# Kernel optimization log

Measured on AMD Instinct MI355X. Metric: run time of the kernel, lower is better.

## Reference

```python
import jax, jax.numpy as jnp
import numpy as np

NUM_ITER = 3  # routing iterations (canonical CapsNet)
EPS = 1e-12


def _conv(x, w, stride):
    return jax.lax.conv_general_dilated(
        x, w, (stride, stride), 'VALID',
        dimension_numbers=('NCHW', 'OIHW', 'NCHW'))


def _squash(t, axis=-1):
    sn = (t * t).sum(axis=axis, keepdims=True)
    return sn / (1.0 + sn) * t / jnp.sqrt(sn + EPS)


def _batchnorm(x, eps=1e-5):
    # fresh BatchNorm2d in training mode: batch stats, weight=1, bias=0, biased var
    m = x.mean((0, 2, 3), keepdims=True)
    v = ((x - m) ** 2).mean((0, 2, 3), keepdims=True)
    return (x - m) * jax.lax.rsqrt(v + eps)


def _branch(x, cw, cb, pw, pb, rw):
    # x: [B,1,H,W]; cw: [128,1,k,k]; pw: [8,32,128,k,k]; rw: [10,R,8,16]
    y = jax.nn.relu(_conv(x, cw, 1) + cb[None, :, None, None])
    y = _batchnorm(y)
    nc, oc = pw.shape[0], pw.shape[1]  # 8 capsules, 32 channels each
    p = _conv(y, pw.reshape(nc * oc, pw.shape[2], pw.shape[3], pw.shape[4]), 2)
    p = p + pb.reshape(-1)[None, :, None, None]          # [B,256,h,w]
    B = p.shape[0]
    u = jnp.transpose(p.reshape(B, nc, -1), (0, 2, 1))   # [B,R,8], R=32*h*w
    u = _squash(u, axis=-1)
    priors = jnp.einsum('bri,nrio->nbro', u, rw)         # [10,B,R,16]
    b = jnp.zeros(priors.shape[:3] + (1,), priors.dtype)  # [10,B,R,1]
    for i in range(NUM_ITER):
        c = jax.nn.softmax(b, axis=2)                    # over route nodes
        v = _squash((c * priors).sum(axis=2, keepdims=True))  # [10,B,1,16]
        if i < NUM_ITER - 1:
            b = b + (priors * v).sum(axis=-1, keepdims=True)
    v = jnp.transpose(v[:, :, 0, :], (1, 0, 2))          # [B,10,16]
    return jnp.sqrt((v * v).sum(-1) + EPS)               # [B,10] capsule lengths


def setup_inputs() -> dict:
    key = jax.random.key(0)
    ks = jax.random.split(key, 16)
    s = 0.05
    return {
        'x': jax.random.normal(ks[0], (256, 1, 28, 28), jnp.float32),
        'conv1_w': jax.random.normal(ks[1], (128, 1, 3, 3), jnp.float32) * s,
        'conv1_b': jnp.zeros((128,), jnp.float32),
        'prim1_w': jax.random.normal(ks[2], (8, 32, 128, 3, 3), jnp.float32) * s,
        'prim1_b': jnp.zeros((8, 32), jnp.float32),
        'digit1_w': jax.random.normal(ks[3], (10, 128, 8, 16), jnp.float32),
        'conv2_w': jax.random.normal(ks[4], (128, 1, 5, 5), jnp.float32) * s,
        'conv2_b': jnp.zeros((128,), jnp.float32),
        'prim2_w': jax.random.normal(ks[5], (8, 32, 128, 5, 5), jnp.float32) * s,
        'prim2_b': jnp.zeros((8, 32), jnp.float32),
        'digit2_w': jax.random.normal(ks[6], (10, 288, 8, 16), jnp.float32),
        'conv3_w': jax.random.normal(ks[7], (128, 1, 9, 9), jnp.float32) * s,
        'conv3_b': jnp.zeros((128,), jnp.float32),
        'prim3_w': jax.random.normal(ks[8], (8, 32, 128, 9, 9), jnp.float32) * s,
        'prim3_b': jnp.zeros((8, 32), jnp.float32),
        'digit3_w': jax.random.normal(ks[9], (10, 1152, 8, 16), jnp.float32),
    }


def reference(x, conv1_w, conv1_b, prim1_w, prim1_b, digit1_w,
              conv2_w, conv2_b, prim2_w, prim2_b, digit2_w,
              conv3_w, conv3_b, prim3_w, prim3_b, digit3_w):
    img = x[:, 0]                                   # [B,28,28]
    B = img.shape[0]
    x3 = img                                        # 28x28
    x2 = img.reshape(B, 14, 2, 14, 2).mean((2, 4))  # 14x14 pyramid level
    x1 = x2.reshape(B, 7, 2, 7, 2).mean((2, 4))     # 7x7 pyramid level
    l1 = _branch(x1[:, None], conv1_w, conv1_b, prim1_w, prim1_b, digit1_w)
    l2 = _branch(x2[:, None], conv2_w, conv2_b, prim2_w, prim2_b, digit2_w)
    l3 = _branch(x3[:, None], conv3_w, conv3_b, prim3_w, prim3_b, digit3_w)
    return jax.nn.softmax(l1 + l2 + l3, axis=-1)    # [B,10]
```

## Files before the change

kernel.cpp:

```cpp
#include <hip/hip_runtime.h>
#include <math.h>

#define SQ_EPS 1e-12f
#define BN_EPS 1e-5f

typedef short short8 __attribute__((ext_vector_type(8)));
typedef float f32x4 __attribute__((ext_vector_type(4)));
typedef unsigned short ushort_t;

__device__ inline unsigned short f2bf(float x) {
    unsigned int u = __float_as_uint(x);
    unsigned int r = (u + 0x7fffu + ((u >> 16) & 1u)) >> 16;
    return (unsigned short)r;
}
__device__ inline float bf2f(unsigned short h) {
    return __uint_as_float(((unsigned int)h) << 16);
}

template<int IH, int IW, int KS, int OH, int OW>
__device__ void conv_body(const float* __restrict__ w, const float* __restrict__ bias,
                          ushort_t* __restrict__ yh, ushort_t* __restrict__ yl,
                          float* __restrict__ partial,
                          int b, int tid, float* s_img, float* s_w, float* s_red) {
    constexpr int KK = KS * KS;
    constexpr int OS = OH * OW;
    for (int i = tid; i < 128 * KK; i += 256) s_w[i] = w[i];
    __syncthreads();
    int c = tid & 127, half = tid >> 7;
    float bias_c = bias[c];
    float bsum = 0.f, bsq = 0.f;
    for (int r = half; r < OH; r += 2) {
        float acc[OW];
        #pragma unroll
        for (int j = 0; j < OW; ++j) acc[j] = bias_c;
        for (int u = 0; u < KS; ++u) {
            float rg[OW + KS - 1];
            #pragma unroll
            for (int j = 0; j < OW + KS - 1; ++j) rg[j] = s_img[(r + u) * IW + j];
            #pragma unroll
            for (int v = 0; v < KS; ++v) {
                float wv = s_w[c * KK + u * KS + v];
                #pragma unroll
                for (int j = 0; j < OW; ++j) acc[j] += wv * rg[j + v];
            }
        }
        #pragma unroll
        for (int j = 0; j < OW; ++j) {
            float val = fmaxf(acc[j], 0.f);
            bsum += val; bsq += val * val;
            unsigned short h = f2bf(val);
            unsigned short lo = f2bf(val - bf2f(h));
            int oidx = ((b * OS) + r * OW + j) * 128 + c;
            yh[oidx] = h; yl[oidx] = lo;
        }
    }
    s_red[tid] = bsum; __syncthreads();
    if (tid < 128) partial[b * 256 + c] = s_red[tid] + s_red[tid + 128];
    __syncthreads();
    s_red[tid] = bsq; __syncthreads();
    if (tid < 128) partial[b * 256 + 128 + c] = s_red[tid] + s_red[tid + 128];
}

__global__ __launch_bounds__(256) void conv_all_kernel(
        const float* __restrict__ img,
        const float* __restrict__ c1w, const float* __restrict__ c1b,
        const float* __restrict__ c2w, const float* __restrict__ c2b,
        const float* __restrict__ c3w, const float* __restrict__ c3b,
        ushort_t* __restrict__ yh1, ushort_t* __restrict__ yl1,
        ushort_t* __restrict__ yh2, ushort_t* __restrict__ yl2,
        ushort_t* __restrict__ yh3, ushort_t* __restrict__ yl3,
        float* __restrict__ partial_base) {
    __shared__ float s_img[784];
    __shared__ float s_tmp[196];
    __shared__ float s_w[128 * 81];
    __shared__ float s_red[256];
    int br = blockIdx.x >> 8, b = blockIdx.x & 255, tid = threadIdx.x;
    const float* im = img + b * 784;
    for (int i = tid; i < 784; i += 256) s_img[i] = im[i];
    __syncthreads();
    if (br <= 1) {
        for (int idx = tid; idx < 196; idx += 256) {
            int i = idx / 14, j = idx % 14;
            s_tmp[idx] = 0.25f * (s_img[(2*i)*28 + 2*j]   + s_img[(2*i)*28 + 2*j + 1] +
                                  s_img[(2*i+1)*28 + 2*j] + s_img[(2*i+1)*28 + 2*j + 1]);
        }
        __syncthreads();
        if (br == 0) {
            for (int idx = tid; idx < 49; idx += 256) {
                int i = idx / 7, j = idx % 7;
                s_img[idx] = 0.25f * (s_tmp[(2*i)*14 + 2*j]   + s_tmp[(2*i)*14 + 2*j + 1] +
                                      s_tmp[(2*i+1)*14 + 2*j] + s_tmp[(2*i+1)*14 + 2*j + 1]);
            }
        } else {
            for (int idx = tid; idx < 196; idx += 256) s_img[idx] = s_tmp[idx];
        }
        __syncthreads();
    }
    if (br == 0)      conv_body<7, 7, 3, 5, 5>(c1w, c1b, yh1, yl1, partial_base, b, tid, s_img, s_w, s_red);
    else if (br == 1) conv_body<14, 14, 5, 10, 10>(c2w, c2b, yh2, yl2, partial_base + 65536, b, tid, s_img, s_w, s_red);
    else              conv_body<28, 28, 9, 20, 20>(c3w, c3b, yh3, yl3, partial_base + 131072, b, tid, s_img, s_w, s_red);
}

__global__ void bn_final_kernel(const float* __restrict__ partial_base, float* __restrict__ bnp_base) {
    int br = blockIdx.x;
    const float* pp = partial_base + br * 65536;
    float* bnp = bnp_base + br * 512;
    float N = (br == 0) ? 6400.f : ((br == 1) ? 25600.f : 102400.f);
    int c = threadIdx.x;
    float s = 0.f, q = 0.f;
    for (int blk = 0; blk < 256; ++blk) {
        s += pp[blk * 256 + c];
        q += pp[blk * 256 + 128 + c];
    }
    float mean = s / N;
    float var = q / N - mean * mean;
    float inv = rsqrtf(var + BN_EPS);
    bnp[256 + c] = inv;
    bnp[384 + c] = -mean * inv;
}

__global__ __launch_bounds__(256) void wtrans_zero_kernel(
        const float* __restrict__ w1, const float* __restrict__ w2,
        const float* __restrict__ w3, const float* __restrict__ bnp_base,
        const float* __restrict__ pb1, const float* __restrict__ pb2,
        const float* __restrict__ pb3,
        ushort_t* __restrict__ wh1, ushort_t* __restrict__ wl1,
        ushort_t* __restrict__ wh2, ushort_t* __restrict__ wl2,
        ushort_t* __restrict__ wh3, ushort_t* __restrict__ wl3,
        float* __restrict__ b1, float* __restrict__ b2, float* __restrict__ b3,
        float* __restrict__ p3zero) {
    __shared__ float tile[128 * 81];
    __shared__ float r2[2];
    int blk = blockIdx.x, tid = threadIdx.x;
    if (blk >= 768) {
        ((float4*)p3zero)[(blk - 768) * 256 + tid] = (float4){0.f, 0.f, 0.f, 0.f};
        return;
    }
    int br = blk >> 8, ch = blk & 255;
    const float* w; const float* pb; ushort_t* wh; ushort_t* wl; float* bf; int KK;
    if (br == 0)      { w = w1; pb = pb1; wh = wh1; wl = wl1; bf = b1; KK = 9;  }
    else if (br == 1) { w = w2; pb = pb2; wh = wh2; wl = wl2; bf = b2; KK = 25; }
    else              { w = w3; pb = pb3; wh = wh3; wl = wl3; bf = b3; KK = 81; }
    const float* bnp = bnp_base + br * 512;
    int n = 128 * KK;
    const float* wrow = w + ch * n;
    for (int i = tid; i < n; i += 256) tile[i] = wrow[i];
    __syncthreads();
    for (int j = tid; j < n; j += 256) {
        int uv = j >> 7, c = j & 127;
        float val = tile[c * KK + uv] * bnp[256 + c];
        unsigned short h = f2bf(val);
        unsigned short lo = f2bf(val - bf2f(h));
        int oidx = uv * 32768 + (ch << 7) + c;
        wh[oidx] = h; wl[oidx] = lo;
    }
    float s = 0.f;
    if (tid < 128) {
        for (int uv = 0; uv < KK; ++uv) s += tile[tid * KK + uv];
        s *= bnp[384 + tid];
    }
    for (int off = 32; off; off >>= 1) s += __shfl_down(s, off);
    if (tid < 128 && (tid & 63) == 0) r2[tid >> 6] = s;
    __syncthreads();
    if (tid == 0) bf[ch] = pb[ch] + r2[0] + r2[1];
}

template<int S, int WO, int IHg, int IWg, int KS, int ZCH>
__device__ void gemm_body(const ushort_t* __restrict__ yh, const ushort_t* __restrict__ yl,
                          const ushort_t* __restrict__ wh, const ushort_t* __restrict__ wl,
                          float* __restrict__ p, int bx, int by, int bz, int tid,
                          ushort_t* Ash, ushort_t* Asl, ushort_t* Bsh, ushort_t* Bsl) {
    int bm = bx * 128, ch0 = by * 128;
    int arow = tid >> 2;
    int c0 = tid & 3;
    int sw0 = (c0 ^ ((arow >> 1) & 3)) * 8;
    int wA0 = arow * 32 + sw0;
    int wA1 = (arow + 64) * 32 + sw0;
    int m0 = bm + arow;
    int b0 = m0 / S, s0 = m0 % S;
    int abase0 = ((b0 * IHg + 2 * (s0 / WO)) * IWg + 2 * (s0 % WO)) * 128 + c0 * 8;
    int m1 = m0 + 64;
    int b1 = m1 / S, s1 = m1 % S;
    int abase1 = ((b1 * IHg + 2 * (s1 / WO)) * IWg + 2 * (s1 % WO)) * 128 + c0 * 8;
    int bbase0 = (ch0 + arow) * 128 + c0 * 8;
    int bbase1 = (ch0 + arow + 64) * 128 + c0 * 8;
    int lane = tid & 63, wid = tid >> 6;
    int wm = wid & 1, wn = wid >> 1;
    int quad = lane >> 4, l16 = lane & 15;
    int aoffL[4], boffL[4];
    #pragma unroll
    for (int mi = 0; mi < 4; ++mi) {
        int row = wm * 64 + mi * 16 + l16;
        aoffL[mi] = row * 32 + ((quad ^ ((row >> 1) & 3)) * 8);
    }
    #pragma unroll
    for (int ni = 0; ni < 4; ++ni) {
        int row = wn * 64 + ni * 16 + l16;
        boffL[ni] = row * 32 + ((quad ^ ((row >> 1) & 3)) * 8);
    }
    f32x4 acc[4][4];
    #pragma unroll
    for (int mi = 0; mi < 4; ++mi)
        #pragma unroll
        for (int ni = 0; ni < 4; ++ni)
            acc[mi][ni] = (f32x4){0.f, 0.f, 0.f, 0.f};

    int kc = bz * ZCH;
    int uv = kc >> 2, ci = kc & 3;
    int u = uv / KS, v = uv - u * KS;
    int aoff = (u * IWg + v) * 128 + (ci << 5);
    int boff = uv * 32768 + (ci << 5);
    int4 a0h = *reinterpret_cast<const int4*>(yh + abase0 + aoff);
    int4 a0l = *reinterpret_cast<const int4*>(yl + abase0 + aoff);
    int4 a1h = *reinterpret_cast<const int4*>(yh + abase1 + aoff);
    int4 a1l = *reinterpret_cast<const int4*>(yl + abase1 + aoff);
    int4 b0h = *reinterpret_cast<const int4*>(wh + bbase0 + boff);
    int4 b0l = *reinterpret_cast<const int4*>(wl + bbase0 + boff);
    int4 b1h = *reinterpret_cast<const int4*>(wh + bbase1 + boff);
    int4 b1l = *reinterpret_cast<const int4*>(wl + bbase1 + boff);

    for (int t = 0; t < ZCH; ++t) {
        __syncthreads();
        *reinterpret_cast<int4*>(&Ash[wA0]) = a0h;
        *reinterpret_cast<int4*>(&Asl[wA0]) = a0l;
        *reinterpret_cast<int4*>(&Ash[wA1]) = a1h;
        *reinterpret_cast<int4*>(&Asl[wA1]) = a1l;
        *reinterpret_cast<int4*>(&Bsh[wA0]) = b0h;
        *reinterpret_cast<int4*>(&Bsl[wA0]) = b0l;
        *reinterpret_cast<int4*>(&Bsh[wA1]) = b1h;
        *reinterpret_cast<int4*>(&Bsl[wA1]) = b1l;
        if (t + 1 < ZCH) {
            ci = (ci + 1) & 3;
            if (ci == 0) { ++uv; ++v; if (v == KS) { v = 0; ++u; } }
            aoff = (u * IWg + v) * 128 + (ci << 5);
            boff = uv * 32768 + (ci << 5);
            a0h = *reinterpret_cast<const int4*>(yh + abase0 + aoff);
            a0l = *reinterpret_cast<const int4*>(yl + abase0 + aoff);
            a1h = *reinterpret_cast<const int4*>(yh + abase1 + aoff);
            a1l = *reinterpret_cast<const int4*>(yl + abase1 + aoff);
            b0h = *reinterpret_cast<const int4*>(wh + bbase0 + boff);
            b0l = *reinterpret_cast<const int4*>(wl + bbase0 + boff);
            b1h = *reinterpret_cast<const int4*>(wh + bbase1 + boff);
            b1l = *reinterpret_cast<const int4*>(wl + bbase1 + boff);
        }
        __syncthreads();
        short8 bh[4], bl[4];
        #pragma unroll
        for (int ni = 0; ni < 4; ++ni) {
            bh[ni] = *reinterpret_cast<const short8*>(&Bsh[boffL[ni]]);
            bl[ni] = *reinterpret_cast<const short8*>(&Bsl[boffL[ni]]);
        }
        #pragma unroll
        for (int mi = 0; mi < 4; ++mi) {
            short8 ah = *reinterpret_cast<const short8*>(&Ash[aoffL[mi]]);
            short8 al = *reinterpret_cast<const short8*>(&Asl[aoffL[mi]]);
            #pragma unroll
            for (int ni = 0; ni < 4; ++ni) {
                acc[mi][ni] = __builtin_amdgcn_mfma_f32_16x16x32_bf16(ah, bh[ni], acc[mi][ni], 0, 0, 0);
                acc[mi][ni] = __builtin_amdgcn_mfma_f32_16x16x32_bf16(al, bh[ni], acc[mi][ni], 0, 0, 0);
                acc[mi][ni] = __builtin_amdgcn_mfma_f32_16x16x32_bf16(ah, bl[ni], acc[mi][ni], 0, 0, 0);
            }
        }
    }
    #pragma unroll
    for (int mi = 0; mi < 4; ++mi)
        #pragma unroll
        for (int ni = 0; ni < 4; ++ni) {
            int col = ch0 + wn * 64 + ni * 16 + l16;
            #pragma unroll
            for (int reg = 0; reg < 4; ++reg) {
                int row = bm + wm * 64 + mi * 16 + quad * 4 + reg;
                atomicAdd(p + (size_t)row * 256 + col, acc[mi][ni][reg]);
            }
        }
}

__global__ __launch_bounds__(256, 3) void gemm3_kernel(
        const ushort_t* __restrict__ yh, const ushort_t* __restrict__ yl,
        const ushort_t* __restrict__ wh, const ushort_t* __restrict__ wl,
        float* __restrict__ p) {
    __shared__ ushort_t Ash[128 * 32], Asl[128 * 32];
    __shared__ ushort_t Bsh[128 * 32], Bsl[128 * 32];
    gemm_body<36, 6, 20, 20, 9, 54>(yh, yl, wh, wl, p,
                                    blockIdx.x, blockIdx.y, blockIdx.z, threadIdx.x,
                                    Ash, Asl, Bsh, Bsl);
}

__global__ __launch_bounds__(256, 3) void gemm21_kernel(
        const ushort_t* __restrict__ yh2, const ushort_t* __restrict__ yl2,
        const ushort_t* __restrict__ wh2, const ushort_t* __restrict__ wl2, float* __restrict__ p2,
        const ushort_t* __restrict__ yh1, const ushort_t* __restrict__ yl1,
        const ushort_t* __restrict__ wh1, const ushort_t* __restrict__ wl1, float* __restrict__ p1) {
    __shared__ ushort_t Ash[128 * 32], Asl[128 * 32];
    __shared__ ushort_t Bsh[128 * 32], Bsl[128 * 32];
    int blk = blockIdx.x, tid = threadIdx.x;
    if (blk < 360) {
        int z = blk / 36, rem = blk % 36, y = rem / 18, x = rem % 18;
        gemm_body<9, 3, 10, 10, 5, 10>(yh2, yl2, wh2, wl2, p2, x, y, z, tid, Ash, Asl, Bsh, Bsl);
    } else {
        int b = blk - 360;
        int z = b / 16, rem = b % 16, y = rem / 8, x = rem % 8;
        gemm_body<4, 2, 5, 5, 3, 4>(yh1, yl1, wh1, wl1, p1, x, y, z, tid, Ash, Asl, Bsh, Bsl);
    }
}

__global__ void squash_all_kernel(const float* __restrict__ p1, const float* __restrict__ p2,
                                  const float* __restrict__ p3,
                                  const float* __restrict__ bias1, const float* __restrict__ bias2,
                                  const float* __restrict__ bias3,
                                  float* __restrict__ u1, float* __restrict__ u2,
                                  float* __restrict__ u3) {
    int blk = blockIdx.x;
    const float* p; const float* bias; float* u; int S;
    if (blk < 128)      { p = p1; bias = bias1; u = u1; S = 4; }
    else if (blk < 416) { p = p2; bias = bias2; u = u2; S = 9;  blk -= 128; }
    else                { p = p3; bias = bias3; u = u3; S = 36; blk -= 416; }
    int idx = blk * 256 + threadIdx.x;
    int o = idx & 31, rest = idx >> 5;
    int s = rest % S, b = rest / S;
    const float* pp = p + (size_t)(b * S + s) * 256 + o;
    float t[8]; float sn = 0.f;
    #pragma unroll
    for (int i = 0; i < 8; ++i) { t[i] = pp[i * 32] + bias[o + i * 32]; sn += t[i] * t[i]; }
    float f = sn / ((1.f + sn) * sqrtf(sn + SQ_EPS));
    float* up = u + (size_t)(b * (32 * S) + o * S + s) * 8;
    float4 w0 = {t[0] * f, t[1] * f, t[2] * f, t[3] * f};
    float4 w1 = {t[4] * f, t[5] * f, t[6] * f, t[7] * f};
    *reinterpret_cast<float4*>(up) = w0;
    *reinterpret_cast<float4*>(up + 4) = w1;
}

__global__ void rwtrans_zero_kernel(const float* __restrict__ w1, const float* __restrict__ w2,
                                    const float* __restrict__ w3,
                                    float* __restrict__ o1, float* __restrict__ o2,
                                    float* __restrict__ o3,
                                    float* __restrict__ p2, float* __restrict__ p1) {
    int blk = blockIdx.x;
    if (blk >= 7840) {
        int zb = blk - 7840;
        if (zb < 576) ((float4*)p2)[zb * 256 + threadIdx.x] = (float4){0.f, 0.f, 0.f, 0.f};
        else          ((float4*)p1)[(zb - 576) * 256 + threadIdx.x] = (float4){0.f, 0.f, 0.f, 0.f};
        return;
    }
    int idx = blk * 256 + threadIdx.x;
    if (idx < 163840) {
        int t = idx;
        int jj = t & 3; t >>= 2;
        int r = t & 127; t >>= 7;
        int g2 = t & 31; int n = t >> 5;
        o1[idx] = w1[(n * 128 + r) * 128 + g2 * 4 + jj];
    } else if (idx < 532480) {
        int t = idx - 163840;
        int jj = t & 3; t >>= 2;
        int r = t % 288; t /= 288;
        int g2 = t & 31; int n = t >> 5;
        o2[idx - 163840] = w2[(n * 288 + r) * 128 + g2 * 4 + jj];
    } else {
        int t = idx - 532480;
        int jj = t & 3; t >>= 2;
        int r = t % 1152; t /= 1152;
        int g2 = t & 31; int n = t >> 5;
        o3[idx - 532480] = w3[(n * 1152 + r) * 128 + g2 * 4 + jj];
    }
}

template<int R>
__device__ void routing_body(const float* __restrict__ u, const float* __restrict__ rwt,
                             float* __restrict__ lens, int n, int b, int tid,
                             unsigned int* pri, float* red, float* vsh, float* sred) {
    constexpr int KMAX = (R + 255) / 256;
    int lane = tid & 63, wv = tid >> 6;
    #pragma unroll
    for (int k = 0; k < KMAX; ++k) {
        int r = tid + k * 256;
        if (r < R) {
            const float4* up = (const float4*)(u + ((size_t)b * R + r) * 8);
            float4 ua = up[0], ub2 = up[1];
            float uu[8] = {ua.x, ua.y, ua.z, ua.w, ub2.x, ub2.y, ub2.z, ub2.w};
            float po[16] = {};
            #pragma unroll
            for (int g2 = 0; g2 < 32; ++g2) {
                float4 w4 = *reinterpret_cast<const float4*>(rwt + (((size_t)n * 32 + g2) * R + r) * 4);
                float ui = uu[g2 >> 2];
                int o0 = (g2 & 3) * 4;
                po[o0 + 0] += ui * w4.x;
                po[o0 + 1] += ui * w4.y;
                po[o0 + 2] += ui * w4.z;
                po[o0 + 3] += ui * w4.w;
            }
            unsigned int d[8];
            #pragma unroll
            for (int j = 0; j < 8; ++j)
                d[j] = (unsigned int)f2bf(po[2*j]) | ((unsigned int)f2bf(po[2*j+1]) << 16);
            int i0 = r * 8 + ((0 ^ (r & 1)) * 4);
            int i1 = r * 8 + ((1 ^ (r & 1)) * 4);
            *reinterpret_cast<uint4*>(pri + i0) = (uint4){d[0], d[1], d[2], d[3]};
            *reinterpret_cast<uint4*>(pri + i1) = (uint4){d[4], d[5], d[6], d[7]};
        }
    }
    __syncthreads();
    float v[16];
    float blog[KMAX];
    #pragma unroll
    for (int k = 0; k < KMAX; ++k) blog[k] = 0.f;
    {
        float sacc[16] = {};
        #pragma unroll
        for (int k = 0; k < KMAX; ++k) {
            int r = tid + k * 256;
            if (r < R) {
                int i0 = r * 8 + ((0 ^ (r & 1)) * 4);
                int i1 = r * 8 + ((1 ^ (r & 1)) * 4);
                uint4 h0 = *reinterpret_cast<const uint4*>(pri + i0);
                uint4 h1 = *reinterpret_cast<const uint4*>(pri + i1);
                unsigned int d[8] = {h0.x, h0.y, h0.z, h0.w, h1.x, h1.y, h1.z, h1.w};
                #pragma unroll
                for (int j = 0; j < 8; ++j) {
                    sacc[2*j]   += bf2f((unsigned short)(d[j] & 0xffffu));
                    sacc[2*j+1] += bf2f((unsigned short)(d[j] >> 16));
                }
            }
        }
        #pragma unroll
        for (int o = 0; o < 16; ++o) {
            float xv = sacc[o];
            for (int off = 32; off; off >>= 1) xv += __shfl_down(xv, off);
            if (lane == 0) red[wv * 16 + o] = xv;
        }
        __syncthreads();
        if (tid < 16) vsh[tid] = (red[tid] + red[16 + tid] + red[32 + tid] + red[48 + tid]) * (1.0f / (float)R);
        __syncthreads();
        if (tid == 0) {
            float sn = 0.f;
            #pragma unroll
            for (int o = 0; o < 16; ++o) sn += vsh[o] * vsh[o];
            float f = sn / ((1.f + sn) * sqrtf(sn + SQ_EPS));
            #pragma unroll
            for (int o = 0; o < 16; ++o) vsh[o] *= f;
        }
        __syncthreads();
        #pragma unroll
        for (int o = 0; o < 16; ++o) v[o] = vsh[o];
        __syncthreads();
    }
    for (int it = 0; it < 2; ++it) {
        float sacc[16] = {};
        float lsum = 0.f;
        #pragma unroll
        for (int k = 0; k < KMAX; ++k) {
            int r = tid + k * 256;
            if (r < R) {
                int i0 = r * 8 + ((0 ^ (r & 1)) * 4);
                int i1 = r * 8 + ((1 ^ (r & 1)) * 4);
                uint4 h0 = *reinterpret_cast<const uint4*>(pri + i0);
                uint4 h1 = *reinterpret_cast<const uint4*>(pri + i1);
                unsigned int d[8] = {h0.x, h0.y, h0.z, h0.w, h1.x, h1.y, h1.z, h1.w};
                float pv[16];
                #pragma unroll
                for (int j = 0; j < 8; ++j) {
                    pv[2*j]   = bf2f((unsigned short)(d[j] & 0xffffu));
                    pv[2*j+1] = bf2f((unsigned short)(d[j] >> 16));
                }
                float dot = 0.f;
                #pragma unroll
                for (int o = 0; o < 16; ++o) dot += pv[o] * v[o];
                blog[k] += dot;
                float e = expf(blog[k]);
                lsum += e;
                #pragma unroll
                for (int o = 0; o < 16; ++o) sacc[o] += e * pv[o];
            }
        }
        for (int off = 32; off; off >>= 1) lsum += __shfl_down(lsum, off);
        if (lane == 0) sred[wv] = lsum;
        #pragma unroll
        for (int o = 0; o < 16; ++o) {
            float xv = sacc[o];
            for (int off = 32; off; off >>= 1) xv += __shfl_down(xv, off);
            if (lane == 0) red[wv * 16 + o] = xv;
        }
        __syncthreads();
        if (tid < 16) {
            float tot = sred[0] + sred[1] + sred[2] + sred[3];
            vsh[tid] = (red[tid] + red[16 + tid] + red[32 + tid] + red[48 + tid]) / tot;
        }
        __syncthreads();
        if (tid == 0) {
            float sn = 0.f;
            #pragma unroll
            for (int o = 0; o < 16; ++o) sn += vsh[o] * vsh[o];
            float f = sn / ((1.f + sn) * sqrtf(sn + SQ_EPS));
            #pragma unroll
            for (int o = 0; o < 16; ++o) vsh[o] *= f;
        }
        __syncthreads();
        #pragma unroll
        for (int o = 0; o < 16; ++o) v[o] = vsh[o];
        __syncthreads();
    }
    if (tid == 0) {
        float sn = 0.f;
        #pragma unroll
        for (int o = 0; o < 16; ++o) sn += v[o] * v[o];
        lens[b * 10 + n] = sqrtf(sn + SQ_EPS);
    }
}

__global__ __launch_bounds__(256, 4) void routing_all_kernel(
        const float* __restrict__ u1, const float* __restrict__ u2, const float* __restrict__ u3,
        const float* __restrict__ rwt1, const float* __restrict__ rwt2,
        const float* __restrict__ rwt3,
        float* __restrict__ l1, float* __restrict__ l2, float* __restrict__ l3) {
    __shared__ unsigned int pri[8 * 1152];
    __shared__ float red[4 * 16];
    __shared__ float vsh[16];
    __shared__ float sred[4];
    int n = blockIdx.x, b = blockIdx.y, br = 2 - blockIdx.z, tid = threadIdx.x;
    if (br == 0)      routing_body<128>(u1, rwt1, l1, n, b, tid, pri, red, vsh, sred);
    else if (br == 1) routing_body<288>(u2, rwt2, l2, n, b, tid, pri, red, vsh, sred);
    else              routing_body<1152>(u3, rwt3, l3, n, b, tid, pri, red, vsh, sred);
}

__global__ void final_softmax_kernel(const float* __restrict__ l1, const float* __restrict__ l2,
                                     const float* __restrict__ l3, float* __restrict__ out) {
    int b = threadIdx.x;
    float v[10]; float mx = -1e30f;
    #pragma unroll
    for (int n = 0; n < 10; ++n) {
        v[n] = l1[b * 10 + n] + l2[b * 10 + n] + l3[b * 10 + n];
        mx = fmaxf(mx, v[n]);
    }
    float s = 0.f;
    #pragma unroll
    for (int n = 0; n < 10; ++n) { v[n] = expf(v[n] - mx); s += v[n]; }
    float inv = 1.f / s;
    #pragma unroll
    for (int n = 0; n < 10; ++n) out[b * 10 + n] = v[n] * inv;
}

extern "C" void kernel_launch(void* const* d_in, const int* in_sizes, int n_in,
                              void* d_out, int out_size, void* d_ws, size_t ws_size,
                              hipStream_t stream) {
    const float* x   = (const float*)d_in[0];
    const float* c1w = (const float*)d_in[1];
    const float* c1b = (const float*)d_in[2];
    const float* p1w = (const float*)d_in[3];
    const float* p1b = (const float*)d_in[4];
    const float* d1w = (const float*)d_in[5];
    const float* c2w = (const float*)d_in[6];
    const float* c2b = (const float*)d_in[7];
    const float* p2w = (const float*)d_in[8];
    const float* p2b = (const float*)d_in[9];
    const float* d2w = (const float*)d_in[10];
    const float* c3w = (const float*)d_in[11];
    const float* c3b = (const float*)d_in[12];
    const float* p3w = (const float*)d_in[13];
    const float* p3b = (const float*)d_in[14];
    const float* d3w = (const float*)d_in[15];

    float* ws = (float*)d_ws;
    float* yh1f  = ws + 62720;
    float* yl1f  = ws + 472320;
    float* yh2f  = ws + 881920;
    float* yl2f  = ws + 2520320;
    float* yh3f  = ws + 4158720;
    float* yl3f  = ws + 10712320;
    float* wh1f  = ws + 17265920;
    float* wl1f  = ws + 17413376;
    float* wh2f  = ws + 17560832;
    float* wl2f  = ws + 17970432;
    float* wh3f  = ws + 18380032;
    float* wl3f  = ws + 19707136;
    float* p3    = ws + 21034240;
    float* bnp1  = ws + 23393536;
    float* bias1 = ws + 23395072;
    float* bias2 = ws + 23395328;
    float* bias3 = ws + 23395584;
    float* l1    = ws + 23395840;
    float* l2    = ws + 23398400;
    float* l3    = ws + 23400960;

    ushort_t* yh1 = (ushort_t*)yh1f; ushort_t* yl1 = (ushort_t*)yl1f;
    ushort_t* yh2 = (ushort_t*)yh2f; ushort_t* yl2 = (ushort_t*)yl2f;
    ushort_t* yh3 = (ushort_t*)yh3f; ushort_t* yl3 = (ushort_t*)yl3f;
    ushort_t* wh1 = (ushort_t*)wh1f; ushort_t* wl1 = (ushort_t*)wl1f;
    ushort_t* wh2 = (ushort_t*)wh2f; ushort_t* wl2 = (ushort_t*)wl2f;
    ushort_t* wh3 = (ushort_t*)wh3f; ushort_t* wl3 = (ushort_t*)wl3f;
    float* u1 = yh1f;
    float* u2 = yh2f;
    float* u3 = yh3f;
    float* p2 = wh3f;
    float* p1 = wl3f;
    float* rwt1 = yl3f;
    float* rwt2 = rwt1 + 163840;
    float* rwt3 = rwt2 + 368640;

    conv_all_kernel<<<768, 256, 0, stream>>>(x, c1w, c1b, c2w, c2b, c3w, c3b,
                                             yh1, yl1, yh2, yl2, yh3, yl3, p3);
    bn_final_kernel<<<3, 128, 0, stream>>>(p3, bnp1);
    wtrans_zero_kernel<<<3072, 256, 0, stream>>>(p1w, p2w, p3w, bnp1, p1b, p2b, p3b,
                                                 wh1, wl1, wh2, wl2, wh3, wl3,
                                                 bias1, bias2, bias3, p3);
    gemm3_kernel<<<dim3(72, 2, 6), 256, 0, stream>>>(yh3, yl3, wh3, wl3, p3);
    rwtrans_zero_kernel<<<8672, 256, 0, stream>>>(d1w, d2w, d3w, rwt1, rwt2, rwt3, p2, p1);
    gemm21_kernel<<<504, 256, 0, stream>>>(yh2, yl2, wh2, wl2, p2, yh1, yl1, wh1, wl1, p1);
    squash_all_kernel<<<1568, 256, 0, stream>>>(p1, p2, p3, bias1, bias2, bias3, u1, u2, u3);
    routing_all_kernel<<<dim3(10, 256, 3), 256, 0, stream>>>(u1, u2, u3, rwt1, rwt2, rwt3, l1, l2, l3);
    final_softmax_kernel<<<1, 256, 0, stream>>>(l1, l2, l3, (float*)d_out);
}
```

Before: 532.9 us.

## Keep routing priors in registers and use transpose-style wave reductions

The routing kernel now keeps each thread's bf16-packed priors in registers rather than a 36 KB shared-memory buffer, which removes LDS traffic and the LDS limit on occupancy. The first routing iteration reuses the fp32 sums from the prior computation. The 16-component wave reductions become a butterfly transpose, squash is computed in parallel across 16 lanes, and fast __expf replaces expf. The cost is higher register pressure, up to 40 packed words per thread for R=1152, which may lower occupancy or cause spills, and there are small numeric differences from the fp32 first pass and __expf.

Measured after the change: 549.9 us. 3.2% more time.

```diff
diff --git a/kernel.cpp b/kernel.cpp
--- a/kernel.cpp
+++ b/kernel.cpp
@@ -367,9 +367,21 @@
 template<int R>
 __device__ void routing_body(const float* __restrict__ u, const float* __restrict__ rwt,
                              float* __restrict__ lens, int n, int b, int tid,
-                             unsigned int* pri, float* red, float* vsh, float* sred) {
+                             float* red, float* vsh, float* sred) {
     constexpr int KMAX = (R + 255) / 256;
+    constexpr float invR = 1.0f / (float)R;
     int lane = tid & 63, wv = tid >> 6;
+
+    unsigned int d[KMAX][8];
+    float a[16];
+    float blog[KMAX];
+    float v[16];
+
+    #pragma unroll
+    for (int o = 0; o < 16; ++o) a[o] = 0.f;
+    #pragma unroll
+    for (int k = 0; k < KMAX; ++k) blog[k] = 0.f;
+
     #pragma unroll
     for (int k = 0; k < KMAX; ++k) {
         int r = tid + k * 256;
@@ -377,7 +389,9 @@
             const float4* up = (const float4*)(u + ((size_t)b * R + r) * 8);
             float4 ua = up[0], ub2 = up[1];
             float uu[8] = {ua.x, ua.y, ua.z, ua.w, ub2.x, ub2.y, ub2.z, ub2.w};
-            float po[16] = {};
+            float po[16];
+            #pragma unroll
+            for (int o = 0; o < 16; ++o) po[o] = 0.f;
             #pragma unroll
             for (int g2 = 0; g2 < 32; ++g2) {
                 float4 w4 = *reinterpret_cast<const float4*>(rwt + (((size_t)n * 32 + g2) * R + r) * 4);
@@ -388,121 +402,91 @@
                 po[o0 + 2] += ui * w4.z;
                 po[o0 + 3] += ui * w4.w;
             }
-            unsigned int d[8];
             #pragma unroll
             for (int j = 0; j < 8; ++j)
-                d[j] = (unsigned int)f2bf(po[2*j]) | ((unsigned int)f2bf(po[2*j+1]) << 16);
-            int i0 = r * 8 + ((0 ^ (r & 1)) * 4);
-            int i1 = r * 8 + ((1 ^ (r & 1)) * 4);
-            *reinterpret_cast<uint4*>(pri + i0) = (uint4){d[0], d[1], d[2], d[3]};
-            *reinterpret_cast<uint4*>(pri + i1) = (uint4){d[4], d[5], d[6], d[7]};
-        }
-    }
-    __syncthreads();
-    float v[16];
-    float blog[KMAX];
-    #pragma unroll
-    for (int k = 0; k < KMAX; ++k) blog[k] = 0.f;
-    {
-        float sacc[16] = {};
-        #pragma unroll
-        for (int k = 0; k < KMAX; ++k) {
-            int r = tid + k * 256;
-            if (r < R) {
-                int i0 = r * 8 + ((0 ^ (r & 1)) * 4);
-                int i1 = r * 8 + ((1 ^ (r & 1)) * 4);
-                uint4 h0 = *reinterpret_cast<const uint4*>(pri + i0);
-                uint4 h1 = *reinterpret_cast<const uint4*>(pri + i1);
-                unsigned int d[8] = {h0.x, h0.y, h0.z, h0.w, h1.x, h1.y, h1.z, h1.w};
-                #pragma unroll
-                for (int j = 0; j < 8; ++j) {
-                    sacc[2*j]   += bf2f((unsigned short)(d[j] & 0xffffu));
-                    sacc[2*j+1] += bf2f((unsigned short)(d[j] >> 16));
+                d[k][j] = (unsigned int)f2bf(po[2*j]) | ((unsigned int)f2bf(po[2*j+1]) << 16);
+            #pragma unroll
+            for (int o = 0; o < 16; ++o) a[o] += po[o];
+        }
+    }
+
+    for (int it = 0; it < 3; ++it) {
+        if (it > 0) {
+            float lsum = 0.f;
+            #pragma unroll
+            for (int o = 0; o < 16; ++o) a[o] = 0.f;
+            #pragma unroll
+            for (int k = 0; k < KMAX; ++k) {
+                int r = tid + k * 256;
+                if (r < R) {
+                    float pv[16];
+                    #pragma unroll
+                    for (int j = 0; j < 8; ++j) {
+                        pv[2*j]   = __uint_as_float(d[k][j] << 16);
+                        pv[2*j+1] = __uint_as_float(d[k][j] & 0xffff0000u);
+                    }
+                    float dt0 = 0.f, dt1 = 0.f, dt2 = 0.f, dt3 = 0.f;
+                    #pragma unroll
+                    for (int o = 0; o < 4; ++o) {
+                        dt0 += pv[o]      * v[o];
+                        dt1 += pv[4 + o]  * v[4 + o];
+                        dt2 += pv[8 + o]  * v[8 + o];
+                        dt3 += pv[12 + o] * v[12 + o];
+                    }
+                    blog[k] += (dt0 + dt1) + (dt2 + dt3);
+                    float e = __expf(blog[k]);
+                    lsum += e;
+                    #pragma unroll
+                    for (int o = 0; o < 16; ++o) a[o] += e * pv[o];
                 }
             }
-        }
-        #pragma unroll
-        for (int o = 0; o < 16; ++o) {
-            float xv = sacc[o];
-            for (int off = 32; off; off >>= 1) xv += __shfl_down(xv, off);
-            if (lane == 0) red[wv * 16 + o] = xv;
-        }
-        __syncthreads();
-        if (tid < 16) vsh[tid] = (red[tid] + red[16 + tid] + red[32 + tid] + red[48 + tid]) * (1.0f / (float)R);
-        __syncthreads();
-        if (tid == 0) {
-            float sn = 0.f;
-            #pragma unroll
-            for (int o = 0; o < 16; ++o) sn += vsh[o] * vsh[o];
-            float f = sn / ((1.f + sn) * sqrtf(sn + SQ_EPS));
-            #pragma unroll
-            for (int o = 0; o < 16; ++o) vsh[o] *= f;
-        }
-        __syncthreads();
-        #pragma unroll
-        for (int o = 0; o < 16; ++o) v[o] = vsh[o];
-        __syncthreads();
-    }
-    for (int it = 0; it < 2; ++it) {
-        float sacc[16] = {};
-        float lsum = 0.f;
-        #pragma unroll
-        for (int k = 0; k < KMAX; ++k) {
-            int r = tid + k * 256;
-            if (r < R) {
-                int i0 = r * 8 + ((0 ^ (r & 1)) * 4);
-                int i1 = r * 8 + ((1 ^ (r & 1)) * 4);
-                uint4 h0 = *reinterpret_cast<const uint4*>(pri + i0);
-                uint4 h1 = *reinterpret_cast<const uint4*>(pri + i1);
-                unsigned int d[8] = {h0.x, h0.y, h0.z, h0.w, h1.x, h1.y, h1.z, h1.w};
-                float pv[16];
-                #pragma unroll
-                for (int j = 0; j < 8; ++j) {
-                    pv[2*j]   = bf2f((unsigned short)(d[j] & 0xffffu));
-                    pv[2*j+1] = bf2f((unsigned short)(d[j] >> 16));
-                }
-                float dot = 0.f;
-                #pragma unroll
-                for (int o = 0; o < 16; ++o) dot += pv[o] * v[o];
-                blog[k] += dot;
-                float e = expf(blog[k]);
-                lsum += e;
-                #pragma unroll
-                for (int o = 0; o < 16; ++o) sacc[o] += e * pv[o];
-            }
-        }
-        for (int off = 32; off; off >>= 1) lsum += __shfl_down(lsum, off);
-        if (lane == 0) sred[wv] = lsum;
-        #pragma unroll
-        for (int o = 0; o < 16; ++o) {
-            float xv = sacc[o];
-            for (int off = 32; off; off >>= 1) xv += __shfl_down(xv, off);
-            if (lane == 0) red[wv * 16 + o] = xv;
-        }
+            lsum += __shfl_xor(lsum, 1);
+            lsum += __shfl_xor(lsum, 2);
+            lsum += __shfl_xor(lsum, 4);
+            lsum += __shfl_xor(lsum, 8);
+            lsum += __shfl_xor(lsum, 16);
+            lsum += __shfl_xor(lsum, 32);
+            if (lane == 0) sred[wv] = lsum;
+        }
+        #pragma unroll
+        for (int k2 = 0; k2 < 4; ++k2) {
+            int m = 1 << k2;
+            int lb = (lane >> k2) & 1;
+            #pragma unroll
+            for (int t = 0; t < (8 >> k2); ++t) {
+                float x0 = a[2 * t], x1 = a[2 * t + 1];
+                float keep = lb ? x1 : x0;
+                float send = lb ? x0 : x1;
+                a[t] = keep + __shfl_xor(send, m);
+            }
+        }
+        float tot = a[0];
+        tot += __shfl_xor(tot, 16);
+        tot += __shfl_xor(tot, 32);
+        if (lane < 16) red[wv * 16 + lane] = tot;
         __syncthreads();
         if (tid < 16) {
-            float tot = sred[0] + sred[1] + sred[2] + sred[3];
-            vsh[tid] = (red[tid] + red[16 + tid] + red[32 + tid] + red[48 + tid]) / tot;
+            float vo = red[tid] + red[16 + tid] + red[32 + tid] + red[48 + tid];
+            float scale = (it == 0) ? invR
+                                    : 1.0f / (sred[0] + sred[1] + sred[2] + sred[3]);
+            vo *= scale;
+            float sn = vo * vo;
+            sn += __shfl_xor(sn, 1);
+            sn += __shfl_xor(sn, 2);
+            sn += __shfl_xor(sn, 4);
+            sn += __shfl_xor(sn, 8);
+            float f = sn / ((1.f + sn) * sqrtf(sn + SQ_EPS));
+            if (it == 2) {
+                if (tid == 0) lens[b * 10 + n] = sqrtf(sn * f * f + SQ_EPS);
+            } else {
+                vsh[tid] = vo * f;
+            }
         }
         __syncthreads();
-        if (tid == 0) {
-            float sn = 0.f;
-            #pragma unroll
-            for (int o = 0; o < 16; ++o) sn += vsh[o] * vsh[o];
-            float f = sn / ((1.f + sn) * sqrtf(sn + SQ_EPS));
-            #pragma unroll
-            for (int o = 0; o < 16; ++o) vsh[o] *= f;
-        }
-        __syncthreads();
-        #pragma unroll
-        for (int o = 0; o < 16; ++o) v[o] = vsh[o];
-        __syncthreads();
-    }
-    if (tid == 0) {
-        float sn = 0.f;
-        #pragma unroll
-        for (int o = 0; o < 16; ++o) sn += v[o] * v[o];
-        lens[b * 10 + n] = sqrtf(sn + SQ_EPS);
+        if (it < 2) {
+            #pragma unroll
+            for (int o = 0; o < 16; ++o) v[o] = vsh[o];
+        }
     }
 }
 
@@ -511,14 +495,13 @@
         const float* __restrict__ rwt1, const float* __restrict__ rwt2,
         const float* __restrict__ rwt3,
         float* __restrict__ l1, float* __restrict__ l2, float* __restrict__ l3) {
-    __shared__ unsigned int pri[8 * 1152];
-    __shared__ float red[4 * 16];
+    __shared__ float red[64];
     __shared__ float vsh[16];
     __shared__ float sred[4];
     int n = blockIdx.x, b = blockIdx.y, br = 2 - blockIdx.z, tid = threadIdx.x;
-    if (br == 0)      routing_body<128>(u1, rwt1, l1, n, b, tid, pri, red, vsh, sred);
-    else if (br == 1) routing_body<288>(u2, rwt2, l2, n, b, tid, pri, red, vsh, sred);
-    else              routing_body<1152>(u3, rwt3, l3, n, b, tid, pri, red, vsh, sred);
+    if (br == 0)      routing_body<128>(u1, rwt1, l1, n, b, tid, red, vsh, sred);
+    else if (br == 1) routing_body<288>(u2, rwt2, l2, n, b, tid, red, vsh, sred);
+    else              routing_body<1152>(u3, rwt3, l3, n, b, tid, red, vsh, sred);
 }
 
 __global__ void final_softmax_kernel(const float* __restrict__ l1, const float* __restrict__ l2,
```
